# Kernel tuning notes

Hardware: AMD Instinct MI355X
Metric: run time of the kernel (lower is better)

Reference implementation:

```python
import jax, jax.numpy as jnp
import numpy as np

N_NODES = 50000
N_EDGES = 800000


def _glorot(key, shape):
    fan_in, fan_out = shape
    lim = float(np.sqrt(6.0 / (fan_in + fan_out)))
    return jax.random.uniform(key, shape, jnp.float32, -lim, lim)


def setup_inputs() -> dict:
    key = jax.random.key(0)
    ks = jax.random.split(key, 8)
    x = jax.random.normal(ks[0], (N_NODES, 2), jnp.float32)
    edge_index = jax.random.randint(ks[1], (2, N_EDGES), 0, N_NODES, jnp.int64)
    edge_weight = jax.random.uniform(ks[2], (N_EDGES,), jnp.float32)
    return {
        "x": x,
        "edge_index": edge_index,
        "edge_weight": edge_weight,
        "W1": _glorot(ks[3], (2, 128)),
        "b1": jnp.zeros((128,), jnp.float32),
        "W2": _glorot(ks[4], (128, 64)),
        "b2": jnp.zeros((64,), jnp.float32),
        "W3": _glorot(ks[5], (64, 1)),
        "b3": jnp.zeros((1,), jnp.float32),
    }


def _gcn_conv(x, W, b, src, dst, ew, n_nodes):
    # PyG GCNConv with normalize=False: out[i] = sum_{e:(j->i)} ew[e] * (x_j @ W) + b
    h = x @ W                       # [N, F_out] tiny GEMM
    msg = h[src] * ew[:, None]      # [E, F_out] gather + scale
    out = jax.ops.segment_sum(msg, dst, num_segments=n_nodes)  # scatter-add
    return out + b


def reference(x, edge_index, edge_weight, W1, b1, W2, b2, W3, b3):
    src, dst = edge_index[0], edge_index[1]  # source_to_target flow: aggregate at dst
    n = x.shape[0]
    h1 = jax.nn.relu(_gcn_conv(x, W1, b1, src, dst, edge_weight, n))
    # dropout is a no-op in eval mode
    h2 = jax.nn.relu(_gcn_conv(h1, W2, b2, src, dst, edge_weight, n))
    h3 = _gcn_conv(h2, W3, b3, src, dst, edge_weight, n)  # [N, 1]
    return h3.squeeze(-1)  # [N]
```

## Files before the change

### kernel.cpp

```cpp
#include <hip/hip_runtime.h>
#include <hip/hip_fp16.h>

#define N_NODES 50000
#define N_EDGES 800000
#define BSHIFT 7
#define NBKT ((N_NODES + 127) >> BSHIFT)
#define CAP 3072
#define P1_EDGES 2048
#define P1_BLOCKS ((N_EDGES + P1_EDGES - 1) / P1_EDGES)
#define BIN_THREADS 512
#define SORT_THREADS 256
#define SORT_LDS_CAP 3072

__global__ void bin_edges(const int* __restrict__ src, const int* __restrict__ dst,
                          const float* __restrict__ ew, int* __restrict__ bcur,
                          unsigned* __restrict__ bpk, unsigned char* __restrict__ bdl) {
    __shared__ unsigned spk[P1_EDGES];
    __shared__ unsigned short sdst[P1_EDGES];
    __shared__ int cnt[NBKT];
    __shared__ int cbase[NBKT];
    int t = threadIdx.x;
    if (t < NBKT) cnt[t] = 0;
    __syncthreads();
    int e0 = blockIdx.x * P1_EDGES;
    for (int k = 0; k < P1_EDGES / BIN_THREADS; k++) {
        int i = k * BIN_THREADS + t;
        int e = e0 + i;
        if (e < N_EDGES) {
            int d = dst[e];
            unsigned hw = (unsigned)__half_as_ushort(__float2half(ew[e]));
            spk[i] = (unsigned)src[e] | (hw << 16);
            sdst[i] = (unsigned short)d;
            atomicAdd(&cnt[d >> BSHIFT], 1);
        }
    }
    __syncthreads();
    if (t < NBKT) {
        int v = cnt[t];
        int base = v ? atomicAdd(&bcur[t], v) : 0;
        cbase[t] = t * CAP + base;
        cnt[t] = 0;
    }
    __syncthreads();
    int nmax = N_EDGES - e0;
    if (nmax > P1_EDGES) nmax = P1_EDGES;
    for (int k = 0; k < P1_EDGES / BIN_THREADS; k++) {
        int i = k * BIN_THREADS + t;
        if (i < nmax) {
            int d = sdst[i];
            int b = d >> BSHIFT;
            int pos = cbase[b] + atomicAdd(&cnt[b], 1);
            bpk[pos] = spk[i];
            bdl[pos] = (unsigned char)(d & 127);
        }
    }
}

__global__ void sort_bucket(const int* __restrict__ bcur, const unsigned* __restrict__ bpk,
                            const unsigned char* __restrict__ bdl,
                            unsigned* __restrict__ sorted, int2* __restrict__ rowspan) {
    __shared__ unsigned spk[SORT_LDS_CAP];
    __shared__ unsigned short sdl[SORT_LDS_CAP];
    __shared__ int nh[128];
    __shared__ int scn[128];
    __shared__ int lcur[128];
    int b = blockIdx.x;
    int t = threadIdx.x;
    int base = b * CAP;
    int n = bcur[b];
    if (n > CAP) n = CAP;
    if (t < 128) nh[t] = 0;
    __syncthreads();
    for (int e = t; e < n; e += SORT_THREADS) {
        spk[e] = bpk[base + e];
        unsigned short d = bdl[base + e];
        sdl[e] = d;
        atomicAdd(&nh[d], 1);
    }
    __syncthreads();
    int v = 0;
    if (t < 128) { v = nh[t]; scn[t] = v; }
    __syncthreads();
    for (int off = 1; off < 128; off <<= 1) {
        int u = (t < 128 && t >= off) ? scn[t - off] : 0;
        __syncthreads();
        if (t < 128) scn[t] += u;
        __syncthreads();
    }
    if (t < 128) {
        int ex = scn[t] - v;
        int node = (b << BSHIFT) + t;
        if (node < N_NODES) rowspan[node] = make_int2(base + ex, base + ex + v);
        nh[t] = ex;
        lcur[t] = 0;
    }
    __syncthreads();
    for (int e = t; e < n; e += SORT_THREADS) {
        int dlow = sdl[e];
        int pos = base + nh[dlow] + atomicAdd(&lcur[dlow], 1);
        sorted[pos] = spk[e];
    }
}

__device__ __forceinline__ float edge_w(unsigned p) {
    return __half2float(__ushort_as_half((unsigned short)(p >> 16)));
}

#define L1_NODES_PER_BLOCK 32
typedef _Float16 f16x8 __attribute__((ext_vector_type(8)));
typedef float f32x4 __attribute__((ext_vector_type(4)));

__global__ void fused_l1(const int2* __restrict__ rowspan, const unsigned* __restrict__ sorted,
                         const float* __restrict__ x, const float* __restrict__ W1,
                         const float* __restrict__ b1, const float* __restrict__ W2,
                         __half* __restrict__ t2) {
    __shared__ __align__(16) __half hls[32][136];
    __shared__ __align__(16) __half w2t[64][136];
    int tid = threadIdx.x;
    int wave = tid >> 6;
    int lane = tid & 63;

    for (int idx = tid; idx < 128 * 64; idx += 256) {
        int k = idx >> 6, nn = idx & 63;
        w2t[nn][k] = __float2half(W2[idx]);
    }
    float w1a = W1[lane],      w1b = W1[128 + lane];
    float w1c = W1[64 + lane], w1d = W1[192 + lane];
    float b1lo = b1[lane], b1hi = b1[64 + lane];

    int sub = lane >> 4;
    int sl  = lane & 15;
    int base = blockIdx.x * L1_NODES_PER_BLOCK + wave * 8;

#pragma unroll
    for (int g = 0; g < 2; g++) {
        int gnode = base + g * 4 + sub;
        float a0 = 0.f, a1 = 0.f;
        if (gnode < N_NODES) {
            int2 sp = rowspan[gnode];
            for (int e = sp.x + sl; e < sp.y; e += 16) {
                unsigned p = sorted[e];
                float w = edge_w(p);
                float2 xv = ((const float2*)x)[p & 0xFFFF];
                a0 = fmaf(w, xv.x, a0);
                a1 = fmaf(w, xv.y, a1);
            }
        }
#pragma unroll
        for (int off = 1; off < 16; off <<= 1) {
            a0 += __shfl_xor(a0, off);
            a1 += __shfl_xor(a1, off);
        }
#pragma unroll
        for (int n = 0; n < 4; n++) {
            float an0 = __shfl(a0, 16 * n);
            float an1 = __shfl(a1, 16 * n);
            float hlo = fmaxf(fmaf(an0, w1a, fmaf(an1, w1b, b1lo)), 0.f);
            float hhi = fmaxf(fmaf(an0, w1c, fmaf(an1, w1d, b1hi)), 0.f);
            int row = wave * 8 + g * 4 + n;
            hls[row][lane] = __float2half(hlo);
            hls[row][64 + lane] = __float2half(hhi);
        }
    }
    __syncthreads();

    int m0 = (wave & 1) * 16;
    int n0 = (wave >> 1) * 32;
    int fr = lane & 15;
    int kb = (lane >> 4) * 8;
    f32x4 acc0 = {0.f, 0.f, 0.f, 0.f};
    f32x4 acc1 = {0.f, 0.f, 0.f, 0.f};
#pragma unroll
    for (int k0 = 0; k0 < 128; k0 += 32) {
        f16x8 av  = *(const f16x8*)&hls[m0 + fr][k0 + kb];
        f16x8 bv0 = *(const f16x8*)&w2t[n0 + fr][k0 + kb];
        f16x8 bv1 = *(const f16x8*)&w2t[n0 + 16 + fr][k0 + kb];
        acc0 = __builtin_amdgcn_mfma_f32_16x16x32_f16(av, bv0, acc0, 0, 0, 0);
        acc1 = __builtin_amdgcn_mfma_f32_16x16x32_f16(av, bv1, acc1, 0, 0, 0);
    }
    int block0 = blockIdx.x * L1_NODES_PER_BLOCK;
#pragma unroll
    for (int r = 0; r < 4; r++) {
        int node = block0 + m0 + (lane >> 4) * 4 + r;
        if (node < N_NODES) {
            t2[node * 64 + n0 + fr]      = __float2half(acc0[r]);
            t2[node * 64 + n0 + 16 + fr] = __float2half(acc1[r]);
        }
    }
}

__global__ void gather2_dot3(const int2* __restrict__ rowspan, const unsigned* __restrict__ sorted,
                             const __half* __restrict__ t2, const float* __restrict__ b2,
                             const float* __restrict__ W3, float* __restrict__ t3) {
    int gtid = blockIdx.x * blockDim.x + threadIdx.x;
    int node = gtid >> 6;
    int lane = threadIdx.x & 63;
    if (node >= N_NODES) return;
    int eg  = lane >> 3;
    int fli = lane & 7;
    int2 sp = rowspan[node];
    float a0 = 0.f, a1 = 0.f, a2 = 0.f, a3 = 0.f, a4 = 0.f, a5 = 0.f, a6 = 0.f, a7 = 0.f;
    int e = sp.x + eg;
    for (; e + 8 < sp.y; e += 16) {
        unsigned p0 = sorted[e];
        unsigned p1 = sorted[e + 8];
        uint4 q0 = *(const uint4*)(t2 + (p0 & 0xFFFF) * 64 + fli * 8);
        uint4 q1 = *(const uint4*)(t2 + (p1 & 0xFFFF) * 64 + fli * 8);
        float w0 = edge_w(p0), w1 = edge_w(p1);
        float2 f;
        f = __half22float2(*(const __half2*)&q0.x); a0 = fmaf(w0, f.x, a0); a1 = fmaf(w0, f.y, a1);
        f = __half22float2(*(const __half2*)&q0.y); a2 = fmaf(w0, f.x, a2); a3 = fmaf(w0, f.y, a3);
        f = __half22float2(*(const __half2*)&q0.z); a4 = fmaf(w0, f.x, a4); a5 = fmaf(w0, f.y, a5);
        f = __half22float2(*(const __half2*)&q0.w); a6 = fmaf(w0, f.x, a6); a7 = fmaf(w0, f.y, a7);
        f = __half22float2(*(const __half2*)&q1.x); a0 = fmaf(w1, f.x, a0); a1 = fmaf(w1, f.y, a1);
        f = __half22float2(*(const __half2*)&q1.y); a2 = fmaf(w1, f.x, a2); a3 = fmaf(w1, f.y, a3);
        f = __half22float2(*(const __half2*)&q1.z); a4 = fmaf(w1, f.x, a4); a5 = fmaf(w1, f.y, a5);
        f = __half22float2(*(const __half2*)&q1.w); a6 = fmaf(w1, f.x, a6); a7 = fmaf(w1, f.y, a7);
    }
    if (e < sp.y) {
        unsigned p = sorted[e];
        uint4 q = *(const uint4*)(t2 + (p & 0xFFFF) * 64 + fli * 8);
        float w = edge_w(p);
        float2 f;
        f = __half22float2(*(const __half2*)&q.x); a0 = fmaf(w, f.x, a0); a1 = fmaf(w, f.y, a1);
        f = __half22float2(*(const __half2*)&q.y); a2 = fmaf(w, f.x, a2); a3 = fmaf(w, f.y, a3);
        f = __half22float2(*(const __half2*)&q.z); a4 = fmaf(w, f.x, a4); a5 = fmaf(w, f.y, a5);
        f = __half22float2(*(const __half2*)&q.w); a6 = fmaf(w, f.x, a6); a7 = fmaf(w, f.y, a7);
    }
#pragma unroll
    for (int off = 8; off < 64; off <<= 1) {
        a0 += __shfl_xor(a0, off); a1 += __shfl_xor(a1, off);
        a2 += __shfl_xor(a2, off); a3 += __shfl_xor(a3, off);
        a4 += __shfl_xor(a4, off); a5 += __shfl_xor(a5, off);
        a6 += __shfl_xor(a6, off); a7 += __shfl_xor(a7, off);
    }
    float4 bA = *(const float4*)(b2 + fli * 8);
    float4 bB = *(const float4*)(b2 + fli * 8 + 4);
    float4 wA = *(const float4*)(W3 + fli * 8);
    float4 wB = *(const float4*)(W3 + fli * 8 + 4);
    float h = fmaxf(a0 + bA.x, 0.f) * wA.x + fmaxf(a1 + bA.y, 0.f) * wA.y +
              fmaxf(a2 + bA.z, 0.f) * wA.z + fmaxf(a3 + bA.w, 0.f) * wA.w +
              fmaxf(a4 + bB.x, 0.f) * wB.x + fmaxf(a5 + bB.y, 0.f) * wB.y +
              fmaxf(a6 + bB.z, 0.f) * wB.z + fmaxf(a7 + bB.w, 0.f) * wB.w;
#pragma unroll
    for (int off = 1; off < 8; off <<= 1) h += __shfl_xor(h, off);
    if (lane == 0) t3[node] = h;
}

__global__ void gather3(const int2* __restrict__ rowspan, const unsigned* __restrict__ sorted,
                        const float* __restrict__ t3, const float* __restrict__ b3,
                        float* __restrict__ out) {
    int gtid = blockIdx.x * blockDim.x + threadIdx.x;
    int wid = gtid >> 6;
    int lane = threadIdx.x & 63;
    int sub = lane >> 4;
    int sl  = lane & 15;
    int node = wid * 4 + sub;
    if (node >= N_NODES) return;
    int2 sp = rowspan[node];
    float acc = 0.f;
    for (int e = sp.x + sl; e < sp.y; e += 16) {
        unsigned p = sorted[e];
        acc = fmaf(edge_w(p), t3[p & 0xFFFF], acc);
    }
#pragma unroll
    for (int off = 1; off < 16; off <<= 1) acc += __shfl_xor(acc, off);
    if (sl == 0) out[node] = acc + b3[0];
}

extern "C" void kernel_launch(void* const* d_in, const int* in_sizes, int n_in,
                              void* d_out, int out_size, void* d_ws, size_t ws_size,
                              hipStream_t stream) {
    const float* x  = (const float*)d_in[0];
    const int*   ei = (const int*)d_in[1];
    const float* ew = (const float*)d_in[2];
    const float* W1 = (const float*)d_in[3];
    const float* b1 = (const float*)d_in[4];
    const float* W2 = (const float*)d_in[5];
    const float* b2 = (const float*)d_in[6];
    const float* W3 = (const float*)d_in[7];
    const float* b3 = (const float*)d_in[8];
    float* out = (float*)d_out;

    const int* src = ei;
    const int* dst = ei + N_EDGES;

    char* p = (char*)d_ws;
    int*  bcur    = (int*)p;            p += NBKT * sizeof(int);
    p = (char*)(((uintptr_t)p + 15) & ~(uintptr_t)15);
    int2* rowspan = (int2*)p;           p += N_NODES * sizeof(int2);
    unsigned* bpk = (unsigned*)p;       p += (long)NBKT * CAP * sizeof(unsigned);
    unsigned char* bdl = (unsigned char*)p; p += (long)NBKT * CAP;
    p = (char*)(((uintptr_t)p + 15) & ~(uintptr_t)15);
    unsigned* sorted  = (unsigned*)p;   p += (long)NBKT * CAP * sizeof(unsigned);
    __half* t2    = (__half*)p;         p += 64L * N_NODES * sizeof(__half);
    float* t3     = (float*)p;          p += N_NODES * sizeof(float);

    hipMemsetAsync(bcur, 0, NBKT * sizeof(int), stream);

    bin_edges<<<P1_BLOCKS, BIN_THREADS, 0, stream>>>(src, dst, ew, bcur, bpk, bdl);
    sort_bucket<<<NBKT, SORT_THREADS, 0, stream>>>(bcur, bpk, bdl, sorted, rowspan);

    fused_l1<<<(N_NODES + L1_NODES_PER_BLOCK - 1) / L1_NODES_PER_BLOCK, 256, 0, stream>>>(
        rowspan, sorted, x, W1, b1, W2, t2);

    gather2_dot3<<<(N_NODES * 64 + 255) / 256, 256, 0, stream>>>(rowspan, sorted, t2, b2, W3, t3);

    gather3<<<((N_NODES + 3) / 4 * 64 + 255) / 256, 256, 0, stream>>>(rowspan, sorted, t3, b3, out);
}
```

Before: 149.2 us.

## Fuse bucket sort with layer-1 aggregation and W2 GEMM into one kernel

```diff
diff --git a/kernel.cpp b/kernel.cpp
--- a/kernel.cpp
+++ b/kernel.cpp
@@ -9,8 +9,7 @@
 #define P1_EDGES 2048
 #define P1_BLOCKS ((N_EDGES + P1_EDGES - 1) / P1_EDGES)
 #define BIN_THREADS 512
-#define SORT_THREADS 256
-#define SORT_LDS_CAP 3072
+#define SL_THREADS 512
 
 __global__ void bin_edges(const int* __restrict__ src, const int* __restrict__ dst,
                           const float* __restrict__ ew, int* __restrict__ bcur,
@@ -56,28 +55,58 @@
     }
 }
 
-__global__ void sort_bucket(const int* __restrict__ bcur, const unsigned* __restrict__ bpk,
-                            const unsigned char* __restrict__ bdl,
-                            unsigned* __restrict__ sorted, int2* __restrict__ rowspan) {
-    __shared__ unsigned spk[SORT_LDS_CAP];
-    __shared__ unsigned short sdl[SORT_LDS_CAP];
-    __shared__ int nh[128];
-    __shared__ int scn[128];
-    __shared__ int lcur[128];
+__device__ __forceinline__ float edge_w(unsigned p) {
+    return __half2float(__ushort_as_half((unsigned short)(p >> 16)));
+}
+
+typedef _Float16 f16x8 __attribute__((ext_vector_type(8)));
+typedef float f32x4 __attribute__((ext_vector_type(4)));
+
+__global__ __launch_bounds__(SL_THREADS) void sort_l1(
+    const int* __restrict__ bcur, const unsigned* __restrict__ bpk,
+    const unsigned char* __restrict__ bdl, const float* __restrict__ x,
+    const float* __restrict__ W1, const float* __restrict__ b1,
+    const float* __restrict__ W2,
+    unsigned* __restrict__ sorted, int2* __restrict__ rowspan,
+    __half* __restrict__ t2) {
+    __shared__ unsigned spk[CAP];
+    __shared__ unsigned short sdl[CAP];
+    __shared__ int nh[128], scn[128], lcur[128];
+    __shared__ float nodeA[128], nodeB[128];
+    __shared__ __align__(16) __half w2t[64][136];
+    __shared__ __align__(16) float w1r0[128];
+    __shared__ __align__(16) float w1r1[128];
+    __shared__ __align__(16) float b1s[128];
+
     int b = blockIdx.x;
     int t = threadIdx.x;
     int base = b * CAP;
     int n = bcur[b];
     if (n > CAP) n = CAP;
-    if (t < 128) nh[t] = 0;
-    __syncthreads();
-    for (int e = t; e < n; e += SORT_THREADS) {
+
+    for (int idx = t; idx < 128 * 64; idx += SL_THREADS) {
+        int k = idx >> 6, nn = idx & 63;
+        w2t[nn][k] = __float2half(W2[idx]);
+    }
+    if (t < 128) {
+        w1r0[t] = W1[t];
+        w1r1[t] = W1[128 + t];
+        b1s[t]  = b1[t];
+        nh[t] = 0;
+        lcur[t] = 0;
+        nodeA[t] = 0.f;
+        nodeB[t] = 0.f;
+    }
+    __syncthreads();
+
+    for (int e = t; e < n; e += SL_THREADS) {
         spk[e] = bpk[base + e];
         unsigned short d = bdl[base + e];
         sdl[e] = d;
         atomicAdd(&nh[d], 1);
     }
     __syncthreads();
+
     int v = 0;
     if (t < 128) { v = nh[t]; scn[t] = v; }
     __syncthreads();
@@ -92,99 +121,59 @@
         int node = (b << BSHIFT) + t;
         if (node < N_NODES) rowspan[node] = make_int2(base + ex, base + ex + v);
         nh[t] = ex;
-        lcur[t] = 0;
-    }
-    __syncthreads();
-    for (int e = t; e < n; e += SORT_THREADS) {
+    }
+    __syncthreads();
+
+    for (int e = t; e < n; e += SL_THREADS) {
+        unsigned p = spk[e];
         int dlow = sdl[e];
         int pos = base + nh[dlow] + atomicAdd(&lcur[dlow], 1);
-        sorted[pos] = spk[e];
-    }
-}
-
-__device__ __forceinline__ float edge_w(unsigned p) {
-    return __half2float(__ushort_as_half((unsigned short)(p >> 16)));
-}
-
-#define L1_NODES_PER_BLOCK 32
-typedef _Float16 f16x8 __attribute__((ext_vector_type(8)));
-typedef float f32x4 __attribute__((ext_vector_type(4)));
-
-__global__ void fused_l1(const int2* __restrict__ rowspan, const unsigned* __restrict__ sorted,
-                         const float* __restrict__ x, const float* __restrict__ W1,
-                         const float* __restrict__ b1, const float* __restrict__ W2,
-                         __half* __restrict__ t2) {
-    __shared__ __align__(16) __half hls[32][136];
-    __shared__ __align__(16) __half w2t[64][136];
-    int tid = threadIdx.x;
-    int wave = tid >> 6;
-    int lane = tid & 63;
-
-    for (int idx = tid; idx < 128 * 64; idx += 256) {
-        int k = idx >> 6, nn = idx & 63;
-        w2t[nn][k] = __float2half(W2[idx]);
-    }
-    float w1a = W1[lane],      w1b = W1[128 + lane];
-    float w1c = W1[64 + lane], w1d = W1[192 + lane];
-    float b1lo = b1[lane], b1hi = b1[64 + lane];
-
-    int sub = lane >> 4;
-    int sl  = lane & 15;
-    int base = blockIdx.x * L1_NODES_PER_BLOCK + wave * 8;
-
-#pragma unroll
-    for (int g = 0; g < 2; g++) {
-        int gnode = base + g * 4 + sub;
-        float a0 = 0.f, a1 = 0.f;
-        if (gnode < N_NODES) {
-            int2 sp = rowspan[gnode];
-            for (int e = sp.x + sl; e < sp.y; e += 16) {
-                unsigned p = sorted[e];
-                float w = edge_w(p);
-                float2 xv = ((const float2*)x)[p & 0xFFFF];
-                a0 = fmaf(w, xv.x, a0);
-                a1 = fmaf(w, xv.y, a1);
-            }
-        }
-#pragma unroll
-        for (int off = 1; off < 16; off <<= 1) {
-            a0 += __shfl_xor(a0, off);
-            a1 += __shfl_xor(a1, off);
-        }
-#pragma unroll
-        for (int n = 0; n < 4; n++) {
-            float an0 = __shfl(a0, 16 * n);
-            float an1 = __shfl(a1, 16 * n);
-            float hlo = fmaxf(fmaf(an0, w1a, fmaf(an1, w1b, b1lo)), 0.f);
-            float hhi = fmaxf(fmaf(an0, w1c, fmaf(an1, w1d, b1hi)), 0.f);
-            int row = wave * 8 + g * 4 + n;
-            hls[row][lane] = __float2half(hlo);
-            hls[row][64 + lane] = __float2half(hhi);
-        }
-    }
-    __syncthreads();
-
-    int m0 = (wave & 1) * 16;
-    int n0 = (wave >> 1) * 32;
+        sorted[pos] = p;
+        float w = edge_w(p);
+        float2 xv = ((const float2*)x)[p & 0xFFFF];
+        atomicAdd(&nodeA[dlow], w * xv.x);
+        atomicAdd(&nodeB[dlow], w * xv.y);
+    }
+    __syncthreads();
+
+    int wave = t >> 6, lane = t & 63;
+    int m0 = wave * 16;
     int fr = lane & 15;
     int kb = (lane >> 4) * 8;
+    float a0 = nodeA[m0 + fr];
+    float a1 = nodeB[m0 + fr];
     f32x4 acc0 = {0.f, 0.f, 0.f, 0.f};
     f32x4 acc1 = {0.f, 0.f, 0.f, 0.f};
+    f32x4 acc2 = {0.f, 0.f, 0.f, 0.f};
+    f32x4 acc3 = {0.f, 0.f, 0.f, 0.f};
 #pragma unroll
     for (int k0 = 0; k0 < 128; k0 += 32) {
-        f16x8 av  = *(const f16x8*)&hls[m0 + fr][k0 + kb];
-        f16x8 bv0 = *(const f16x8*)&w2t[n0 + fr][k0 + kb];
-        f16x8 bv1 = *(const f16x8*)&w2t[n0 + 16 + fr][k0 + kb];
+        f16x8 av;
+#pragma unroll
+        for (int j = 0; j < 8; j++) {
+            int k = k0 + kb + j;
+            float h = fmaxf(fmaf(a0, w1r0[k], fmaf(a1, w1r1[k], b1s[k])), 0.f);
+            av[j] = (_Float16)h;
+        }
+        f16x8 bv0 = *(const f16x8*)&w2t[ 0 + fr][k0 + kb];
+        f16x8 bv1 = *(const f16x8*)&w2t[16 + fr][k0 + kb];
+        f16x8 bv2 = *(const f16x8*)&w2t[32 + fr][k0 + kb];
+        f16x8 bv3 = *(const f16x8*)&w2t[48 + fr][k0 + kb];
         acc0 = __builtin_amdgcn_mfma_f32_16x16x32_f16(av, bv0, acc0, 0, 0, 0);
         acc1 = __builtin_amdgcn_mfma_f32_16x16x32_f16(av, bv1, acc1, 0, 0, 0);
-    }
-    int block0 = blockIdx.x * L1_NODES_PER_BLOCK;
+        acc2 = __builtin_amdgcn_mfma_f32_16x16x32_f16(av, bv2, acc2, 0, 0, 0);
+        acc3 = __builtin_amdgcn_mfma_f32_16x16x32_f16(av, bv3, acc3, 0, 0, 0);
+    }
+    int rowb = (b << BSHIFT) + m0 + (lane >> 4) * 4;
 #pragma unroll
     for (int r = 0; r < 4; r++) {
-        int node = block0 + m0 + (lane >> 4) * 4 + r;
+        int node = rowb + r;
         if (node < N_NODES) {
-            t2[node * 64 + n0 + fr]      = __float2half(acc0[r]);
-            t2[node * 64 + n0 + 16 + fr] = __float2half(acc1[r]);
+            __half* o = t2 + node * 64 + fr;
+            o[0]  = __float2half(acc0[r]);
+            o[16] = __float2half(acc1[r]);
+            o[32] = __float2half(acc2[r]);
+            o[48] = __float2half(acc3[r]);
         }
     }
 }
@@ -299,10 +288,8 @@
     hipMemsetAsync(bcur, 0, NBKT * sizeof(int), stream);
 
     bin_edges<<<P1_BLOCKS, BIN_THREADS, 0, stream>>>(src, dst, ew, bcur, bpk, bdl);
-    sort_bucket<<<NBKT, SORT_THREADS, 0, stream>>>(bcur, bpk, bdl, sorted, rowspan);
-
-    fused_l1<<<(N_NODES + L1_NODES_PER_BLOCK - 1) / L1_NODES_PER_BLOCK, 256, 0, stream>>>(
-        rowspan, sorted, x, W1, b1, W2, t2);
+
+    sort_l1<<<NBKT, SL_THREADS, 0, stream>>>(bcur, bpk, bdl, x, W1, b1, W2, sorted, rowspan, t2);
 
     gather2_dot3<<<(N_NODES * 64 + 255) / 256, 256, 0, stream>>>(rowspan, sorted, t2, b2, W3, t3);
 
```

New measurement: 146.8 us. Within noise of the previous version (-1.6%).
